# Performance work log

Hardware: AMD Instinct MI355X
Metric: run time of the kernel (lower is better)

Reference implementation:

```python
import jax, jax.numpy as jnp
import numpy as np

H = 128  # hidden width of the PINN MLP


def _mlp_scalar(pt, W0, b0, W1, b1, W2, b2, W3, b3):
    # pt: [2] -> scalar u(x, y); tanh MLP as used in PINN solid-mechanics nets
    h = jnp.tanh(pt @ W0 + b0)
    h = jnp.tanh(h @ W1 + b1)
    h = jnp.tanh(h @ W2 + b2)
    return (h @ W3 + b3)[0]


def setup_inputs() -> dict:
    key = jax.random.key(0)
    ks = jax.random.split(key, 6)
    N = 131072
    # Xavier-ish scaling so tanh stays in its smooth regime
    X = jax.random.normal(ks[0], (N, 2), dtype=jnp.float32)
    W0 = jax.random.normal(ks[1], (2, H), dtype=jnp.float32) * (1.0 / np.sqrt(2.0))
    b0 = jnp.zeros((H,), dtype=jnp.float32)
    W1 = jax.random.normal(ks[2], (H, H), dtype=jnp.float32) * (1.0 / np.sqrt(H))
    b1 = jnp.zeros((H,), dtype=jnp.float32)
    W2 = jax.random.normal(ks[3], (H, H), dtype=jnp.float32) * (1.0 / np.sqrt(H))
    b2 = jnp.zeros((H,), dtype=jnp.float32)
    W3 = jax.random.normal(ks[4], (H, 1), dtype=jnp.float32) * (1.0 / np.sqrt(H))
    b3 = jnp.zeros((1,), dtype=jnp.float32)
    return {"X": X, "W0": W0, "b0": b0, "W1": W1, "b1": b1,
            "W2": W2, "b2": b2, "W3": W3, "b3": b3}


def reference(X, W0, b0, W1, b1, W2, b2, W3, b3):
    # Per-point Hessian of u w.r.t. (x, y). Each collocation point is
    # independent, so TF's batched gradient-of-sum equals the per-point
    # derivative; forward-over-reverse (jacfwd o jacrev) vmapped over N is
    # the efficient fused form of the two nested GradientTapes.
    f = lambda pt: _mlp_scalar(pt, W0, b0, W1, b1, W2, b2, W3, b3)
    hess = jax.vmap(jax.jacfwd(jax.jacrev(f)))(X)  # [N, 2, 2]
    du_dxx = hess[:, 0, 0][:, None]  # [N, 1]
    du_dxy = hess[:, 0, 1][:, None]  # [N, 1]
    du_dyy = hess[:, 1, 1][:, None]  # [N, 1]
    return (du_dxx, du_dxy, du_dyy)
```

## Files before the change

### kernel.cpp

```cpp
#include <hip/hip_runtime.h>

#define H   128
#define P   32
#define NT  512

typedef _Float16 v8h __attribute__((ext_vector_type(8)));
typedef __fp16   h2  __attribute__((ext_vector_type(2)));
typedef float    v4f __attribute__((ext_vector_type(4)));
typedef float    v2f __attribute__((ext_vector_type(2)));

union PK4 { h2 h[4]; uint4 u; };
union PK2 { h2 h[2]; uint2 u; };

__device__ __forceinline__ int soct(int pl, int p, int o) {
    return ((pl * P + p) * 16 + (o ^ (p & 15))) << 3;
}

__global__ void wt_convert(const float* __restrict__ W1,
                           const float* __restrict__ W2,
                           _Float16* __restrict__ ws) {
    const int t = blockIdx.x * 64 + threadIdx.x;
    const int l = t >> 13;
    const int r = t & 8191;
    const int oct = r >> 9;
    const int rem = r & 511;
    const int j  = rem >> 2;
    const int wp = rem & 3;
    const int k  = oct * 8 + 2 * wp;
    const float* __restrict__ W = l ? W2 : W1;
    const float a = W[k * H + j];
    const float b = W[(k + 1) * H + j];
    union { h2 h; unsigned u; } q;
    q.h = __builtin_amdgcn_cvt_pkrtz(a, b);
    ((unsigned*)ws)[t] = q.u;
}

__device__ __forceinline__ v2f tanh_d2_p(v2f z, v2f& g1, v2f& g2) {
    v2f r;
    r.x = __builtin_amdgcn_rcpf(__expf(2.f * z.x) + 1.f);
    r.y = __builtin_amdgcn_rcpf(__expf(2.f * z.y) + 1.f);
    const v2f a = -2.f * r + 1.f;
    g1 = 1.f - a * a;
    g2 = -2.f * (a * g1);
    return a;
}

__global__ __launch_bounds__(NT, 4)
void pinn_hess_mfma(const float* __restrict__ X,
                    const float* __restrict__ W0, const float* __restrict__ b0,
                    const _Float16* __restrict__ Wt,
                    const float* __restrict__ b1, const float* __restrict__ b2,
                    const float* __restrict__ W3,
                    float* __restrict__ out, int N)
{
    __shared__ _Float16 sS[6 * P * H];
    __shared__ _Float16 sW[16 * H * 8];

    const int tid   = threadIdx.x;
    const int wave  = tid >> 6;
    const int phalf = wave & 1;
    const int jquad = wave >> 1;
    const int lane  = tid & 63;
    const int quad  = lane >> 4;
    const int l15   = lane & 15;
    const int pbase = blockIdx.x * P;
    const int pmy   = phalf * 16 + l15;

    {
        const int p = tid >> 4, o = tid & 15;
        const float x = X[2 * (pbase + p)];
        const float y = X[2 * (pbase + p) + 1];
        float wxv[8], wyv[8], bv[8];
        *(float4*)&wxv[0] = *(const float4*)&W0[o * 8];
        *(float4*)&wxv[4] = *(const float4*)&W0[o * 8 + 4];
        *(float4*)&wyv[0] = *(const float4*)&W0[H + o * 8];
        *(float4*)&wyv[4] = *(const float4*)&W0[H + o * 8 + 4];
        *(float4*)&bv[0]  = *(const float4*)&b0[o * 8];
        *(float4*)&bv[4]  = *(const float4*)&b0[o * 8 + 4];
        PK4 q[6];
        #pragma unroll
        for (int hp = 0; hp < 4; ++hp) {
            const v2f wx = {wxv[2*hp], wxv[2*hp+1]};
            const v2f wy = {wyv[2*hp], wyv[2*hp+1]};
            const v2f bb = {bv[2*hp],  bv[2*hp+1]};
            v2f g1, g2;
            const v2f a = tanh_d2_p(x * wx + y * wy + bb, g1, g2);
            const v2f gx = g2 * wx;
            const v2f r0 = a,        r1 = g1 * wx,  r2 = g1 * wy;
            const v2f r3 = gx * wx,  r4 = gx * wy,  r5 = (g2 * wy) * wy;
            q[0].h[hp] = __builtin_amdgcn_cvt_pkrtz(r0.x, r0.y);
            q[1].h[hp] = __builtin_amdgcn_cvt_pkrtz(r1.x, r1.y);
            q[2].h[hp] = __builtin_amdgcn_cvt_pkrtz(r2.x, r2.y);
            q[3].h[hp] = __builtin_amdgcn_cvt_pkrtz(r3.x, r3.y);
            q[4].h[hp] = __builtin_amdgcn_cvt_pkrtz(r4.x, r4.y);
            q[5].h[hp] = __builtin_amdgcn_cvt_pkrtz(r5.x, r5.y);
        }
        #pragma unroll
        for (int pl = 0; pl < 6; ++pl)
            *(uint4*)&sS[soct(pl, p, o)] = q[pl].u;
    }

    for (int layer = 0; layer < 2; ++layer) {
        {
            const v8h* src = (const v8h*)(Wt + layer * 16 * H * 8);
            v8h*       dst = (v8h*)sW;
            #pragma unroll
            for (int i = 0; i < 4; ++i)
                dst[tid + i * NT] = src[tid + i * NT];
        }
        __syncthreads();

        v4f C[6][2];
        #pragma unroll
        for (int pl = 0; pl < 6; ++pl) { C[pl][0] = (v4f){0,0,0,0}; C[pl][1] = (v4f){0,0,0,0}; }

        #pragma unroll
        for (int kc = 0; kc < 4; ++kc) {
            const int oct = kc * 4 + quad;
            const v8h A0 = *(const v8h*)&sW[(oct * H + jquad * 32 + l15)      * 8];
            const v8h A1 = *(const v8h*)&sW[(oct * H + jquad * 32 + 16 + l15) * 8];
            #pragma unroll
            for (int pl = 0; pl < 6; ++pl) {
                const v8h B = *(const v8h*)&sS[soct(pl, pmy, oct)];
                C[pl][0] = __builtin_amdgcn_mfma_f32_16x16x32_f16(A0, B, C[pl][0], 0, 0, 0);
                C[pl][1] = __builtin_amdgcn_mfma_f32_16x16x32_f16(A1, B, C[pl][1], 0, 0, 0);
            }
        }
        __syncthreads();

        if (layer == 0) {
            #pragma unroll
            for (int mt = 0; mt < 2; ++mt) {
                const int j0 = jquad * 32 + mt * 16 + quad * 4;
                const float4 bv = *(const float4*)&b1[j0];
                PK2 q[6];
                #pragma unroll
                for (int hp = 0; hp < 2; ++hp) {
                    const v2f zb = hp ? (v2f){C[0][mt][2], C[0][mt][3]}
                                      : (v2f){C[0][mt][0], C[0][mt][1]};
                    const v2f bb = hp ? (v2f){bv.z, bv.w} : (v2f){bv.x, bv.y};
                    const v2f tx = hp ? (v2f){C[1][mt][2], C[1][mt][3]}
                                      : (v2f){C[1][mt][0], C[1][mt][1]};
                    const v2f ty = hp ? (v2f){C[2][mt][2], C[2][mt][3]}
                                      : (v2f){C[2][mt][0], C[2][mt][1]};
                    const v2f cx = hp ? (v2f){C[3][mt][2], C[3][mt][3]}
                                      : (v2f){C[3][mt][0], C[3][mt][1]};
                    const v2f cm = hp ? (v2f){C[4][mt][2], C[4][mt][3]}
                                      : (v2f){C[4][mt][0], C[4][mt][1]};
                    const v2f cy = hp ? (v2f){C[5][mt][2], C[5][mt][3]}
                                      : (v2f){C[5][mt][0], C[5][mt][1]};
                    v2f g1, g2;
                    const v2f a  = tanh_d2_p(zb + bb, g1, g2);
                    const v2f gx = g2 * tx;
                    const v2f s0 = a,        s1 = g1 * tx,          s2 = g1 * ty;
                    const v2f s3 = gx * tx + g1 * cx;
                    const v2f s4 = gx * ty + g1 * cm;
                    const v2f s5 = (g2 * ty) * ty + g1 * cy;
                    q[0].h[hp] = __builtin_amdgcn_cvt_pkrtz(s0.x, s0.y);
                    q[1].h[hp] = __builtin_amdgcn_cvt_pkrtz(s1.x, s1.y);
                    q[2].h[hp] = __builtin_amdgcn_cvt_pkrtz(s2.x, s2.y);
                    q[3].h[hp] = __builtin_amdgcn_cvt_pkrtz(s3.x, s3.y);
                    q[4].h[hp] = __builtin_amdgcn_cvt_pkrtz(s4.x, s4.y);
                    q[5].h[hp] = __builtin_amdgcn_cvt_pkrtz(s5.x, s5.y);
                }
                const int ob = j0 >> 3;
                const int ho = (quad & 1) * 4;
                #pragma unroll
                for (int pl = 0; pl < 6; ++pl)
                    *(uint2*)&sS[soct(pl, pmy, ob) + ho] = q[pl].u;
            }
        } else {
            v2f axx = {0.f, 0.f}, axy = {0.f, 0.f}, ayy = {0.f, 0.f};
            #pragma unroll
            for (int mt = 0; mt < 2; ++mt) {
                const int j0 = jquad * 32 + mt * 16 + quad * 4;
                const float4 bv = *(const float4*)&b2[j0];
                const float4 wv = *(const float4*)&W3[j0];
                #pragma unroll
                for (int hp = 0; hp < 2; ++hp) {
                    const v2f zb = hp ? (v2f){C[0][mt][2], C[0][mt][3]}
                                      : (v2f){C[0][mt][0], C[0][mt][1]};
                    const v2f bb = hp ? (v2f){bv.z, bv.w} : (v2f){bv.x, bv.y};
                    const v2f w3 = hp ? (v2f){wv.z, wv.w} : (v2f){wv.x, wv.y};
                    const v2f tx = hp ? (v2f){C[1][mt][2], C[1][mt][3]}
                                      : (v2f){C[1][mt][0], C[1][mt][1]};
                    const v2f ty = hp ? (v2f){C[2][mt][2], C[2][mt][3]}
                                      : (v2f){C[2][mt][0], C[2][mt][1]};
                    const v2f cx = hp ? (v2f){C[3][mt][2], C[3][mt][3]}
                                      : (v2f){C[3][mt][0], C[3][mt][1]};
                    const v2f cm = hp ? (v2f){C[4][mt][2], C[4][mt][3]}
                                      : (v2f){C[4][mt][0], C[4][mt][1]};
                    const v2f cy = hp ? (v2f){C[5][mt][2], C[5][mt][3]}
                                      : (v2f){C[5][mt][0], C[5][mt][1]};
                    v2f g1, g2;
                    tanh_d2_p(zb + bb, g1, g2);
                    const v2f gx = g2 * tx;
                    axx = axx + w3 * (gx * tx + g1 * cx);
                    axy = axy + w3 * (gx * ty + g1 * cm);
                    ayy = ayy + w3 * ((g2 * ty) * ty + g1 * cy);
                }
            }
            float oxx = axx.x + axx.y, oxy = axy.x + axy.y, oyy = ayy.x + ayy.y;
            oxx += __shfl_xor(oxx, 16); oxx += __shfl_xor(oxx, 32);
            oxy += __shfl_xor(oxy, 16); oxy += __shfl_xor(oxy, 32);
            oyy += __shfl_xor(oyy, 16); oyy += __shfl_xor(oyy, 32);
            float* sRed = (float*)sW;
            if (quad == 0) {
                sRed[0 * 128 + jquad * 32 + pmy] = oxx;
                sRed[1 * 128 + jquad * 32 + pmy] = oxy;
                sRed[2 * 128 + jquad * 32 + pmy] = oyy;
            }
            __syncthreads();
            if (tid < 96) {
                const int c = tid >> 5, p = tid & 31;
                float acc = 0.f;
                #pragma unroll
                for (int jq = 0; jq < 4; ++jq)
                    acc += sRed[c * 128 + jq * 32 + p];
                out[c * N + pbase + p] = acc;
            }
        }
    }
}

extern "C" void kernel_launch(void* const* d_in, const int* in_sizes, int n_in,
                              void* d_out, int out_size, void* d_ws, size_t ws_size,
                              hipStream_t stream) {
    const float* X  = (const float*)d_in[0];
    const float* W0 = (const float*)d_in[1];
    const float* b0 = (const float*)d_in[2];
    const float* W1 = (const float*)d_in[3];
    const float* b1 = (const float*)d_in[4];
    const float* W2 = (const float*)d_in[5];
    const float* b2 = (const float*)d_in[6];
    const float* W3 = (const float*)d_in[7];

    const int N = in_sizes[0] / 2;
    float* out = (float*)d_out;
    _Float16* ws = (_Float16*)d_ws;

    hipLaunchKernelGGL(wt_convert, dim3(256), dim3(64), 0, stream, W1, W2, ws);

    hipLaunchKernelGGL(pinn_hess_mfma, dim3(N / P), dim3(NT), 0, stream,
                       X, W0, b0, ws, b1, b2, W3, out, N);
}
```

Measured before the change: 134.4 us.

## Load weight fragments directly from global into registers, dropping LDS weight staging

The per-layer copy of the fp16 weight matrix into shared memory is removed. Each wave now loads its MFMA A-fragments straight from global memory (expected to hit L2) into registers, double-buffering two k-steps ahead. This cuts the block's LDS footprint so more blocks can be resident per CU, and the final reduction scratch now reuses the activation buffer. Launch bounds are raised to ask for 6 blocks per CU, which may force register caps or spills and makes the MFMAs depend on global load latency.

```diff
diff --git a/kernel.cpp b/kernel.cpp
--- a/kernel.cpp
+++ b/kernel.cpp
@@ -45,7 +45,7 @@
     return a;
 }
 
-__global__ __launch_bounds__(NT, 4)
+__global__ __launch_bounds__(NT, 6)
 void pinn_hess_mfma(const float* __restrict__ X,
                     const float* __restrict__ W0, const float* __restrict__ b0,
                     const _Float16* __restrict__ Wt,
@@ -54,7 +54,6 @@
                     float* __restrict__ out, int N)
 {
     __shared__ _Float16 sS[6 * P * H];
-    __shared__ _Float16 sW[16 * H * 8];
 
     const int tid   = threadIdx.x;
     const int wave  = tid >> 6;
@@ -100,32 +99,41 @@
             *(uint4*)&sS[soct(pl, p, o)] = q[pl].u;
     }
 
+    const int aoff = quad * H + jquad * 32 + l15;
+
     for (int layer = 0; layer < 2; ++layer) {
-        {
-            const v8h* src = (const v8h*)(Wt + layer * 16 * H * 8);
-            v8h*       dst = (v8h*)sW;
-            #pragma unroll
-            for (int i = 0; i < 4; ++i)
-                dst[tid + i * NT] = src[tid + i * NT];
-        }
+        const v8h* __restrict__ Ag = (const v8h*)(Wt + layer * (16 * H * 8));
+
+        v8h Aa0 = Ag[aoff];
+        v8h Aa1 = Ag[aoff + 16];
+        v8h Ab0 = Ag[aoff + 4 * H];
+        v8h Ab1 = Ag[aoff + 4 * H + 16];
+
         __syncthreads();
 
         v4f C[6][2];
         #pragma unroll
         for (int pl = 0; pl < 6; ++pl) { C[pl][0] = (v4f){0,0,0,0}; C[pl][1] = (v4f){0,0,0,0}; }
 
-        #pragma unroll
-        for (int kc = 0; kc < 4; ++kc) {
+        auto kstep = [&](const v8h A0, const v8h A1, const int kc) {
             const int oct = kc * 4 + quad;
-            const v8h A0 = *(const v8h*)&sW[(oct * H + jquad * 32 + l15)      * 8];
-            const v8h A1 = *(const v8h*)&sW[(oct * H + jquad * 32 + 16 + l15) * 8];
             #pragma unroll
             for (int pl = 0; pl < 6; ++pl) {
                 const v8h B = *(const v8h*)&sS[soct(pl, pmy, oct)];
                 C[pl][0] = __builtin_amdgcn_mfma_f32_16x16x32_f16(A0, B, C[pl][0], 0, 0, 0);
                 C[pl][1] = __builtin_amdgcn_mfma_f32_16x16x32_f16(A1, B, C[pl][1], 0, 0, 0);
             }
-        }
+        };
+
+        kstep(Aa0, Aa1, 0);
+        Aa0 = Ag[aoff + 8 * H];
+        Aa1 = Ag[aoff + 8 * H + 16];
+        kstep(Ab0, Ab1, 1);
+        Ab0 = Ag[aoff + 12 * H];
+        Ab1 = Ag[aoff + 12 * H + 16];
+        kstep(Aa0, Aa1, 2);
+        kstep(Ab0, Ab1, 3);
+
         __syncthreads();
 
         if (layer == 0) {
@@ -204,7 +212,7 @@
             oxx += __shfl_xor(oxx, 16); oxx += __shfl_xor(oxx, 32);
             oxy += __shfl_xor(oxy, 16); oxy += __shfl_xor(oxy, 32);
             oyy += __shfl_xor(oyy, 16); oyy += __shfl_xor(oyy, 32);
-            float* sRed = (float*)sW;
+            float* sRed = (float*)sS;
             if (quad == 0) {
                 sRed[0 * 128 + jquad * 32 + pmy] = oxx;
                 sRed[1 * 128 + jquad * 32 + pmy] = oxy;
```

Result: slower. 166.1 us (+23.6%).
